# Performance work log

Hardware: AMD Instinct MI355X
Metric: run time of the kernel (lower is better)

The kernel has to match this reference:

```python
import jax, jax.numpy as jnp
import numpy as np

N = 50000
E = 800000
D_IN = 1000
D_H2 = 128  # h_dim * multiple
D_H = 16


def gat_conv(x, src, dst, W, attn_l, attn_r, bias, n):
    """DGL-style GATConv (no dropout, no activation). Returns [n, H, F]."""
    H, F = attn_l.shape
    feat = (x @ W).reshape(n, H, F)                      # [N,H,F]
    el = jnp.sum(feat * attn_l[None], axis=-1)           # [N,H]
    er = jnp.sum(feat * attn_r[None], axis=-1)           # [N,H]
    e = jax.nn.leaky_relu(el[src] + er[dst], 0.2)        # [E,H]
    emax = jax.ops.segment_max(e, dst, num_segments=n)   # [N,H] per-dst softmax max
    ee = jnp.exp(e - emax[dst])                          # [E,H]
    denom = jax.ops.segment_sum(ee, dst, num_segments=n) # [N,H]
    alpha = ee / denom[dst]                              # [E,H]
    msg = feat[src] * alpha[..., None]                   # [E,H,F]
    out = jax.ops.segment_sum(msg, dst, num_segments=n)  # [N,H,F]
    return out + bias.reshape(1, H, F)


def setup_inputs() -> dict:
    key = jax.random.key(0)
    ks = jax.random.split(key, 24)
    rn = lambda k, shp, s=0.05: (jax.random.normal(k, shp, dtype=jnp.float32) * s)
    inp = {
        "x": rn(ks[0], (N, D_IN), 1.0),
        "src": jax.random.randint(ks[1], (E,), 0, N, dtype=jnp.int32),
        "dst": jax.random.randint(ks[2], (E,), 0, N, dtype=jnp.int32),
        "W1": rn(ks[3], (D_IN, D_H2)),
        "al1": rn(ks[4], (1, D_H2)),
        "ar1": rn(ks[5], (1, D_H2)),
        "b1": jnp.zeros((D_H2,), jnp.float32),
        "W2": rn(ks[6], (D_H2, 2 * D_H2)),
        "al2": rn(ks[7], (2, D_H2)),
        "ar2": rn(ks[8], (2, D_H2)),
        "b2": jnp.zeros((2 * D_H2,), jnp.float32),
        "Wm": rn(ks[9], (D_H2, 2 * D_H)),
        "alm": rn(ks[10], (2, D_H)),
        "arm": rn(ks[11], (2, D_H)),
        "bm": jnp.zeros((2 * D_H,), jnp.float32),
        "Wv": rn(ks[12], (D_H2, 2 * D_H)),
        "alv": rn(ks[13], (2, D_H)),
        "arv": rn(ks[14], (2, D_H)),
        "bv": jnp.zeros((2 * D_H,), jnp.float32),
        "eps": rn(ks[15], (N, D_H), 1.0),
    }
    return inp


def reference(x, src, dst, W1, al1, ar1, b1, W2, al2, ar2, b2,
              Wm, alm, arm, bm, Wv, alv, arv, bv, eps):
    n = x.shape[0]
    o = gat_conv(x, src, dst, W1, al1, ar1, b1, n).mean(-2)           # [N,128]
    o = gat_conv(o, src, dst, W2, al2, ar2, b2, n).mean(-2) + o       # residual
    mean = gat_conv(o, src, dst, Wm, alm, arm, bm, n).mean(-2)        # [N,16]
    var = jnp.exp(gat_conv(o, src, dst, Wv, alv, arv, bv, n).mean(-2))
    z = mean + jnp.sqrt(var) * eps                                    # reparameterize
    return z, mean, var
```

## Files before the change

### kernel.cpp

```cpp
#include <hip/hip_runtime.h>
#include <hip/hip_bf16.h>
#include <math.h>

typedef unsigned short u16;
typedef unsigned int u32;
typedef __attribute__((ext_vector_type(8))) __bf16 bf16x8;
typedef __attribute__((ext_vector_type(4))) float f32x4;
typedef __attribute__((ext_vector_type(4))) u32 u32x4;

#define NNODES 50000
#define NEDGES 800000

__device__ __forceinline__ float bf2f(u16 u) {
    union { u32 i; float f; } v; v.i = ((u32)u) << 16; return v.f;
}
__device__ __forceinline__ u16 f2bf(float x) {
    union { float f; u32 i; } v; v.f = x;
    u32 r = v.i + 0x7fffu + ((v.i >> 16) & 1u);
    return (u16)(r >> 16);
}
__device__ __forceinline__ float lrelu(float x) { return x >= 0.f ? x : 0.2f * x; }

__global__ __launch_bounds__(256) void k_zero2(int* a, int* b, int count) {
    int i = blockIdx.x * 256 + threadIdx.x;
    if (i < count) { a[i] = 0; b[i] = 0; }
}

__global__ __launch_bounds__(256) void k_count(const int* __restrict__ dst, int* __restrict__ counts, int e) {
    int i = blockIdx.x * 256 + threadIdx.x;
    if (i < e) atomicAdd(&counts[dst[i]], 1);
}

__global__ __launch_bounds__(256) void k_scan1(const int* __restrict__ counts, int* __restrict__ row_ptr,
                                               int* __restrict__ bsums, int n) {
    __shared__ int tmp[256];
    int t = threadIdx.x, i = blockIdx.x * 256 + t;
    int v = (i < n) ? counts[i] : 0;
    tmp[t] = v; __syncthreads();
    for (int off = 1; off < 256; off <<= 1) {
        int x = 0; if (t >= off) x = tmp[t - off];
        __syncthreads(); tmp[t] += x; __syncthreads();
    }
    if (i < n) row_ptr[i] = tmp[t] - v;
    if (t == 255) bsums[blockIdx.x] = tmp[255];
}

__global__ __launch_bounds__(256) void k_scan2(int* bsums, int nb) {
    __shared__ int tmp[256];
    int t = threadIdx.x;
    int v = (t < nb) ? bsums[t] : 0;
    tmp[t] = v; __syncthreads();
    for (int off = 1; off < 256; off <<= 1) {
        int x = 0; if (t >= off) x = tmp[t - off];
        __syncthreads(); tmp[t] += x; __syncthreads();
    }
    if (t < nb) bsums[t] = tmp[t] - v;
}

__global__ __launch_bounds__(256) void k_scan3(int* __restrict__ row_ptr, const int* __restrict__ bsums,
                                               int n, int total) {
    int i = blockIdx.x * 256 + threadIdx.x;
    if (i < n) row_ptr[i] += bsums[blockIdx.x];
    if (i == 0) row_ptr[n] = total;
}

__global__ __launch_bounds__(256) void k_fill(const int* __restrict__ src, const int* __restrict__ dst,
                                              const int* __restrict__ row_ptr, int* __restrict__ cursor,
                                              int* __restrict__ esrc, int e) {
    int i = blockIdx.x * 256 + threadIdx.x;
    if (i < e) {
        int d = dst[i];
        int p = row_ptr[d] + atomicAdd(&cursor[d], 1);
        esrc[p] = src[i];
    }
}

__global__ __launch_bounds__(256) void k_prep(const float* __restrict__ W1, const float* __restrict__ W2,
                                              const float* __restrict__ Wm, const float* __restrict__ Wv,
                                              const float* __restrict__ al2, const float* __restrict__ ar2,
                                              const float* __restrict__ b2,
                                              u16* __restrict__ W1t, u16* __restrict__ Wct,
                                              u16* __restrict__ Bmvt,
                                              float* __restrict__ ul, float* __restrict__ ur,
                                              float* __restrict__ bmean) {
    int b = blockIdx.x, t = threadIdx.x;
    if (b < 500) {
        int i = b * 256 + t;
        int k = i >> 7, n = i & 127;
        W1t[(size_t)n * 1000 + k] = f2bf(W1[i]);
    } else if (b < 628) {
        int i = (b - 500) * 256 + t;
        int f = i >> 8, c = i & 255, h = c >> 7, k = c & 127;
        Wct[i] = f2bf(0.5f * W2[(size_t)k * 256 + h * 128 + f]);
    } else if (b == 628) {
        int h = t >> 7, k = t & 127;
        const float* wrow = W2 + (size_t)k * 256 + h * 128;
        const float* alh = al2 + h * 128;
        const float* arh = ar2 + h * 128;
        float sl = 0.f, sr = 0.f;
        for (int f = 0; f < 128; f += 4) {
            f32x4 w = *(const f32x4*)(wrow + f);
            f32x4 a = *(const f32x4*)(alh + f);
            f32x4 r = *(const f32x4*)(arh + f);
#pragma unroll
            for (int q = 0; q < 4; q++) { sl += w[q] * a[q]; sr += w[q] * r[q]; }
        }
        ul[t] = sl; ur[t] = sr;
        if (t < 128) bmean[t] = 0.5f * (b2[t] + b2[128 + t]);
    } else {
        for (int i = t; i < 64 * 128; i += 256) {
            int c = i >> 7, k = i & 127;
            Bmvt[i] = f2bf(c < 32 ? Wm[(size_t)k * 32 + c] : Wv[(size_t)k * 32 + (c - 32)]);
        }
    }
}

__device__ __forceinline__ void load_af(const float* __restrict__ arow, int k0, int K, bf16x8& a) {
    if (k0 + 8 <= K) {
        f32x4 a0 = *(const f32x4*)(arow + k0);
        f32x4 a1 = *(const f32x4*)(arow + k0 + 4);
#pragma unroll
        for (int j = 0; j < 4; j++) { a[j] = (__bf16)a0[j]; a[4 + j] = (__bf16)a1[j]; }
    } else {
#pragma unroll
        for (int j = 0; j < 8; j++) a[j] = (__bf16)0.f;
    }
}
__device__ __forceinline__ void load_af(const u16* __restrict__ arow, int k0, int K, bf16x8& a) {
    if (k0 + 8 <= K) a = *(const bf16x8*)(arow + k0);
    else {
#pragma unroll
        for (int j = 0; j < 8; j++) a[j] = (__bf16)0.f;
    }
}

template <typename AT, int MODE>
__global__ __launch_bounds__(256) void k_gemm_tiled(const AT* __restrict__ A, const u16* __restrict__ Bt,
                                                    u16* __restrict__ C, int M, int Nn, int K,
                                                    const float* __restrict__ bias,
                                                    const u16* __restrict__ resid,
                                                    const float* __restrict__ al,
                                                    const float* __restrict__ ar,
                                                    float* __restrict__ el, float* __restrict__ er) {
    __shared__ __align__(16) u16 lb[2][128 * 40];
    const int tid = threadIdx.x;
    const int wave = tid >> 6, lane = tid & 63;
    const int m = lane & 15, quad = lane >> 4;
    const int row0 = blockIdx.x * 64 + wave * 16;
    const int col0 = blockIdx.y * 128;

    f32x4 acc[8];
#pragma unroll
    for (int t = 0; t < 8; t++)
#pragma unroll
        for (int r = 0; r < 4; r++) acc[t][r] = 0.f;

    int arr = row0 + m; if (arr > M - 1) arr = M - 1;
    const AT* arow = A + (size_t)arr * K;
    const int scol = tid & 127;
    const int sseg = (tid >> 7) * 16;
    const u16* bcol = Bt + (size_t)(col0 + scol) * K;

    const int nsteps = (K + 31) >> 5;

#pragma unroll
    for (int p = 0; p < 2; ++p) {
        int kl = sseg + p * 8;
        u32x4 v = 0;
        if (kl < K) v = *(const u32x4*)(bcol + kl);
        *(u32x4*)&lb[0][scol * 40 + kl] = v;
    }
    bf16x8 acur, anext;
    load_af(arow, quad * 8, K, acur);
    __syncthreads();

    for (int s = 0; s < nsteps; ++s) {
        const int buf = s & 1;
        if (s + 1 < nsteps) {
            const int k0n = (s + 1) * 32;
            load_af(arow, k0n + quad * 8, K, anext);
#pragma unroll
            for (int p = 0; p < 2; ++p) {
                int kl = sseg + p * 8;
                u32x4 v = 0;
                if (k0n + kl < K) v = *(const u32x4*)(bcol + k0n + kl);
                *(u32x4*)&lb[buf ^ 1][scol * 40 + kl] = v;
            }
        }
#pragma unroll
        for (int t = 0; t < 8; ++t) {
            bf16x8 b = *(const bf16x8*)&lb[buf][(t * 16 + m) * 40 + quad * 8];
            acc[t] = __builtin_amdgcn_mfma_f32_16x16x32_bf16(acur, b, acc[t], 0, 0, 0);
        }
        acur = anext;
        __syncthreads();
    }

#pragma unroll
    for (int r = 0; r < 4; r++) {
        int row = row0 + quad * 4 + r;
        if (MODE == 0) {
            float pe = 0.f, pr = 0.f;
#pragma unroll
            for (int t = 0; t < 8; t++) {
                float a = acc[t][r];
                int c = col0 + t * 16 + m;
                pe += a * al[c]; pr += a * ar[c];
            }
#pragma unroll
            for (int off = 8; off; off >>= 1) { pe += __shfl_xor(pe, off); pr += __shfl_xor(pr, off); }
            if (m == 0 && row < M) { el[row] = pe; er[row] = pr; }
        }
#pragma unroll
        for (int t = 0; t < 8; t++) {
            int col = col0 + t * 16 + m;
            if (row < M) {
                float v = acc[t][r];
                if (MODE == 1) v += bias[col] + bf2f(resid[(size_t)row * Nn + col]);
                C[(size_t)row * Nn + col] = f2bf(v);
            }
        }
    }
}

__global__ __launch_bounds__(64) void k_gemmmv(const u16* __restrict__ A, const u16* __restrict__ Bt,
                                               u16* __restrict__ featm, u16* __restrict__ featv,
                                               const float* __restrict__ alm, const float* __restrict__ arm,
                                               const float* __restrict__ alv, const float* __restrict__ arv,
                                               float* __restrict__ elm, float* __restrict__ erm,
                                               float* __restrict__ elv, float* __restrict__ erv, int M) {
    int row0 = blockIdx.x * 16;
    int lane = threadIdx.x;
    int m = lane & 15, quad = lane >> 4;
    f32x4 acc[4];
#pragma unroll
    for (int t = 0; t < 4; t++)
#pragma unroll
        for (int r = 0; r < 4; r++) acc[t][r] = 0.f;

    const u16* arow = A + (size_t)(row0 + m) * 128 + quad * 8;
#pragma unroll
    for (int s = 0; s < 4; ++s) {
        bf16x8 a = *(const bf16x8*)(arow + s * 32);
#pragma unroll
        for (int t = 0; t < 4; t++) {
            bf16x8 b = *(const bf16x8*)(Bt + (size_t)(t * 16 + m) * 128 + s * 32 + quad * 8);
            acc[t] = __builtin_amdgcn_mfma_f32_16x16x32_bf16(a, b, acc[t], 0, 0, 0);
        }
    }
#pragma unroll
    for (int r = 0; r < 4; r++) {
        int row = row0 + quad * 4 + r;
#pragma unroll
        for (int t = 0; t < 4; t++) {
            float a = acc[t][r];
            const float* alp = (t < 2) ? alm : alv;
            const float* arp = (t < 2) ? arm : arv;
            float pe = a * alp[(t & 1) * 16 + m];
            float pr = a * arp[(t & 1) * 16 + m];
#pragma unroll
            for (int off = 8; off; off >>= 1) { pe += __shfl_xor(pe, off); pr += __shfl_xor(pr, off); }
            if (m == 0 && row < M) {
                float* elp = (t < 2) ? elm : elv;
                float* erp = (t < 2) ? erm : erv;
                elp[row * 2 + (t & 1)] = pe; erp[row * 2 + (t & 1)] = pr;
            }
            if (row < M) {
                u16 v = f2bf(a);
                if (t < 2) featm[(size_t)row * 32 + t * 16 + m] = v;
                else       featv[(size_t)row * 32 + (t - 2) * 16 + m] = v;
            }
        }
    }
}

__global__ __launch_bounds__(256) void k_agg1(const int* __restrict__ row_ptr, const int* __restrict__ esrc,
                                              const u16* __restrict__ feat, const float* __restrict__ el,
                                              const float* __restrict__ er, const float* __restrict__ bias,
                                              const float* __restrict__ ul, const float* __restrict__ ur,
                                              u16* __restrict__ o_bf, float* __restrict__ el2,
                                              float* __restrict__ er2, int n) {
    int node = blockIdx.x * 4 + (threadIdx.x >> 6);
    if (node >= n) return;
    int lane = threadIdx.x & 63;
    int beg = row_ptr[node], end = row_ptr[node + 1];
    float erd = er[node];
    float mx = -3.0e38f;
    for (int i = beg + lane; i < end; i += 64) mx = fmaxf(mx, el[esrc[i]]);
#pragma unroll
    for (int off = 32; off; off >>= 1) mx = fmaxf(mx, __shfl_xor(mx, off));
    float me = (end > beg) ? lrelu(mx + erd) : 0.f;
    float acc0 = 0.f, acc1 = 0.f, den = 0.f;
    for (int base = beg; base < end; base += 64) {
        int i = base + lane;
        float w = 0.f; int s = 0;
        if (i < end) { s = esrc[i]; w = expf(lrelu(el[s] + erd) - me); }
        den += w;
        int cnt = min(64, end - base);
        int j = 0;
        for (; j + 4 <= cnt; j += 4) {
            float w0 = __shfl(w, j), w1 = __shfl(w, j + 1), w2 = __shfl(w, j + 2), w3 = __shfl(w, j + 3);
            int s0 = __shfl(s, j), s1 = __shfl(s, j + 1), s2 = __shfl(s, j + 2), s3 = __shfl(s, j + 3);
            u32 p0 = ((const u32*)(feat + (size_t)s0 * 128))[lane];
            u32 p1 = ((const u32*)(feat + (size_t)s1 * 128))[lane];
            u32 p2 = ((const u32*)(feat + (size_t)s2 * 128))[lane];
            u32 p3 = ((const u32*)(feat + (size_t)s3 * 128))[lane];
            acc0 += w0 * bf2f((u16)(p0 & 0xffff)) + w1 * bf2f((u16)(p1 & 0xffff))
                  + w2 * bf2f((u16)(p2 & 0xffff)) + w3 * bf2f((u16)(p3 & 0xffff));
            acc1 += w0 * bf2f((u16)(p0 >> 16)) + w1 * bf2f((u16)(p1 >> 16))
                  + w2 * bf2f((u16)(p2 >> 16)) + w3 * bf2f((u16)(p3 >> 16));
        }
        for (; j < cnt; ++j) {
            float wj = __shfl(w, j);
            int sj = __shfl(s, j);
            u32 pv = ((const u32*)(feat + (size_t)sj * 128))[lane];
            acc0 += wj * bf2f((u16)(pv & 0xffff));
            acc1 += wj * bf2f((u16)(pv >> 16));
        }
    }
#pragma unroll
    for (int off = 32; off; off >>= 1) den += __shfl_xor(den, off);
    float inv = (den > 0.f) ? 1.f / den : 0.f;
    float o0 = acc0 * inv + bias[2 * lane];
    float o1 = acc1 * inv + bias[2 * lane + 1];
#pragma unroll
    for (int h = 0; h < 2; ++h) {
        float pe = o0 * ul[h * 128 + 2 * lane] + o1 * ul[h * 128 + 2 * lane + 1];
        float pr = o0 * ur[h * 128 + 2 * lane] + o1 * ur[h * 128 + 2 * lane + 1];
#pragma unroll
        for (int off = 32; off; off >>= 1) { pe += __shfl_xor(pe, off); pr += __shfl_xor(pr, off); }
        if (lane == 0) { el2[node * 2 + h] = pe; er2[node * 2 + h] = pr; }
    }
    u32 pv = (u32)f2bf(o0) | ((u32)f2bf(o1) << 16);
    ((u32*)(o_bf + (size_t)node * 128))[lane] = pv;
}

__global__ __launch_bounds__(256) void k_agg2o(const int* __restrict__ row_ptr, const int* __restrict__ esrc,
                                               const u16* __restrict__ o_in, const float* __restrict__ el,
                                               const float* __restrict__ er, u16* __restrict__ agg, int n) {
    int node = blockIdx.x * 4 + (threadIdx.x >> 6);
    if (node >= n) return;
    int lane = threadIdx.x & 63;
    int beg = row_ptr[node], end = row_ptr[node + 1];
    float er0 = er[node * 2], er1 = er[node * 2 + 1];
    float mx0 = -3.0e38f, mx1 = -3.0e38f;
    for (int i = beg + lane; i < end; i += 64) {
        int s = esrc[i];
        float2 e2 = *(const float2*)(el + 2 * s);
        mx0 = fmaxf(mx0, e2.x); mx1 = fmaxf(mx1, e2.y);
    }
#pragma unroll
    for (int off = 32; off; off >>= 1) { mx0 = fmaxf(mx0, __shfl_xor(mx0, off)); mx1 = fmaxf(mx1, __shfl_xor(mx1, off)); }
    float me0 = (end > beg) ? lrelu(mx0 + er0) : 0.f;
    float me1 = (end > beg) ? lrelu(mx1 + er1) : 0.f;
    float a00 = 0.f, a01 = 0.f, a10 = 0.f, a11 = 0.f, d0 = 0.f, d1 = 0.f;
    for (int base = beg; base < end; base += 64) {
        int i = base + lane;
        float w0 = 0.f, w1 = 0.f; int s = 0;
        if (i < end) {
            s = esrc[i];
            float2 e2 = *(const float2*)(el + 2 * s);
            w0 = expf(lrelu(e2.x + er0) - me0);
            w1 = expf(lrelu(e2.y + er1) - me1);
        }
        d0 += w0; d1 += w1;
        int cnt = min(64, end - base);
        int j = 0;
        for (; j + 4 <= cnt; j += 4) {
            float w0a = __shfl(w0, j), w0b = __shfl(w0, j + 1), w0c = __shfl(w0, j + 2), w0d = __shfl(w0, j + 3);
            float w1a = __shfl(w1, j), w1b = __shfl(w1, j + 1), w1c = __shfl(w1, j + 2), w1d = __shfl(w1, j + 3);
            int sa = __shfl(s, j), sb = __shfl(s, j + 1), sc = __shfl(s, j + 2), sd = __shfl(s, j + 3);
            u32 pa = ((const u32*)(o_in + (size_t)sa * 128))[lane];
            u32 pb = ((const u32*)(o_in + (size_t)sb * 128))[lane];
            u32 pc = ((const u32*)(o_in + (size_t)sc * 128))[lane];
            u32 pd = ((const u32*)(o_in + (size_t)sd * 128))[lane];
            float la = bf2f((u16)(pa & 0xffff)), ha = bf2f((u16)(pa >> 16));
            float lb = bf2f((u16)(pb & 0xffff)), hb = bf2f((u16)(pb >> 16));
            float lc = bf2f((u16)(pc & 0xffff)), hc = bf2f((u16)(pc >> 16));
            float ld = bf2f((u16)(pd & 0xffff)), hd = bf2f((u16)(pd >> 16));
            a00 += w0a * la + w0b * lb + w0c * lc + w0d * ld;
            a01 += w0a * ha + w0b * hb + w0c * hc + w0d * hd;
            a10 += w1a * la + w1b * lb + w1c * lc + w1d * ld;
            a11 += w1a * ha + w1b * hb + w1c * hc + w1d * hd;
        }
        for (; j < cnt; ++j) {
            float w0j = __shfl(w0, j), w1j = __shfl(w1, j);
            int sj = __shfl(s, j);
            u32 pv = ((const u32*)(o_in + (size_t)sj * 128))[lane];
            float lo = bf2f((u16)(pv & 0xffff)), hi = bf2f((u16)(pv >> 16));
            a00 += w0j * lo; a01 += w0j * hi;
            a10 += w1j * lo; a11 += w1j * hi;
        }
    }
#pragma unroll
    for (int off = 32; off; off >>= 1) { d0 += __shfl_xor(d0, off); d1 += __shfl_xor(d1, off); }
    float i0 = (d0 > 0.f) ? 1.f / d0 : 0.f, i1 = (d1 > 0.f) ? 1.f / d1 : 0.f;
    u32 p0 = (u32)f2bf(a00 * i0) | ((u32)f2bf(a01 * i0) << 16);
    u32 p1 = (u32)f2bf(a10 * i1) | ((u32)f2bf(a11 * i1) << 16);
    u32* aw = (u32*)(agg + (size_t)node * 256);
    aw[lane] = p0;
    aw[64 + lane] = p1;
}

__global__ __launch_bounds__(256) void k_aggmv(const int* __restrict__ row_ptr, const int* __restrict__ esrc,
                                               const u16* __restrict__ featm, const u16* __restrict__ featv,
                                               const float* __restrict__ elm, const float* __restrict__ erm,
                                               const float* __restrict__ elv, const float* __restrict__ erv,
                                               const float* __restrict__ bm, const float* __restrict__ bv,
                                               const float* __restrict__ eps, float* __restrict__ out, int n) {
    int node = blockIdx.x * 4 + (threadIdx.x >> 6);
    if (node >= n) return;
    int lane = threadIdx.x & 63;
    int f = lane & 15, h = (lane >> 4) & 1, tbl = lane >> 5;
    int beg = row_ptr[node], end = row_ptr[node + 1];
    float erm0 = erm[2 * node], erm1 = erm[2 * node + 1];
    float erv0 = erv[2 * node], erv1 = erv[2 * node + 1];
    float mm0 = -3.0e38f, mm1 = -3.0e38f, mv0 = -3.0e38f, mv1 = -3.0e38f;
    for (int i = beg + lane; i < end; i += 64) {
        int s = esrc[i];
        float2 em = *(const float2*)(elm + 2 * s);
        float2 ev = *(const float2*)(elv + 2 * s);
        mm0 = fmaxf(mm0, em.x); mm1 = fmaxf(mm1, em.y);
        mv0 = fmaxf(mv0, ev.x); mv1 = fmaxf(mv1, ev.y);
    }
#pragma unroll
    for (int off = 32; off; off >>= 1) {
        mm0 = fmaxf(mm0, __shfl_xor(mm0, off)); mm1 = fmaxf(mm1, __shfl_xor(mm1, off));
        mv0 = fmaxf(mv0, __shfl_xor(mv0, off)); mv1 = fmaxf(mv1, __shfl_xor(mv1, off));
    }
    float mem0 = (end > beg) ? lrelu(mm0 + erm0) : 0.f;
    float mem1 = (end > beg) ? lrelu(mm1 + erm1) : 0.f;
    float mev0 = (end > beg) ? lrelu(mv0 + erv0) : 0.f;
    float mev1 = (end > beg) ? lrelu(mv1 + erv1) : 0.f;

    const u16* ftp = tbl ? featv : featm;
    const int fidx = h * 16 + f;
    float accv = 0.f;
    float dm0 = 0.f, dm1 = 0.f, dv0 = 0.f, dv1 = 0.f;
    for (int base = beg; base < end; base += 64) {
        int i = base + lane;
        float wm0 = 0.f, wm1 = 0.f, wv0 = 0.f, wv1 = 0.f; int s = 0;
        if (i < end) {
            s = esrc[i];
            float2 em = *(const float2*)(elm + 2 * s);
            float2 ev = *(const float2*)(elv + 2 * s);
            wm0 = expf(lrelu(em.x + erm0) - mem0);
            wm1 = expf(lrelu(em.y + erm1) - mem1);
            wv0 = expf(lrelu(ev.x + erv0) - mev0);
            wv1 = expf(lrelu(ev.y + erv1) - mev1);
        }
        dm0 += wm0; dm1 += wm1; dv0 += wv0; dv1 += wv1;
        int cnt = min(64, end - base);
        for (int j = 0; j < cnt; ++j) {
            int sj = __shfl(s, j);
            float bm0 = __shfl(wm0, j);
            float bm1 = __shfl(wm1, j);
            float bv0 = __shfl(wv0, j);
            float bv1 = __shfl(wv1, j);
            float wj = tbl ? (h ? bv1 : bv0) : (h ? bm1 : bm0);
            accv += wj * bf2f(ftp[(size_t)sj * 32 + fidx]);
        }
    }
#pragma unroll
    for (int off = 32; off; off >>= 1) {
        dm0 += __shfl_xor(dm0, off); dm1 += __shfl_xor(dm1, off);
        dv0 += __shfl_xor(dv0, off); dv1 += __shfl_xor(dv1, off);
    }
    float den = tbl ? (h ? dv1 : dv0) : (h ? dm1 : dm0);
    float inv = (den > 0.f) ? 1.f / den : 0.f;
    float biasc = tbl ? bv[fidx] : bm[fidx];
    float outc = accv * inv + biasc;
    float hm = 0.5f * (outc + __shfl_xor(outc, 16));
    float meanv = __shfl(hm, f);
    float varp = __shfl(hm, 32 + f);
    if (lane < 16) {
        float var = expf(varp);
        float z = meanv + sqrtf(var) * eps[(size_t)node * 16 + f];
        size_t base = (size_t)node * 16 + f;
        out[base] = z;
        out[(size_t)NNODES * 16 + base] = meanv;
        out[(size_t)2 * NNODES * 16 + base] = var;
    }
}

extern "C" void kernel_launch(void* const* d_in, const int* in_sizes, int n_in,
                              void* d_out, int out_size, void* d_ws, size_t ws_size,
                              hipStream_t stream) {
    const int N = NNODES, E = NEDGES;
    const float* x   = (const float*)d_in[0];
    const int* src   = (const int*)d_in[1];
    const int* dst   = (const int*)d_in[2];
    const float* W1  = (const float*)d_in[3];
    const float* al1 = (const float*)d_in[4];
    const float* ar1 = (const float*)d_in[5];
    const float* b1  = (const float*)d_in[6];
    const float* W2  = (const float*)d_in[7];
    const float* al2 = (const float*)d_in[8];
    const float* ar2 = (const float*)d_in[9];
    const float* b2  = (const float*)d_in[10];
    const float* Wm  = (const float*)d_in[11];
    const float* alm = (const float*)d_in[12];
    const float* arm = (const float*)d_in[13];
    const float* bm  = (const float*)d_in[14];
    const float* Wv  = (const float*)d_in[15];
    const float* alv = (const float*)d_in[16];
    const float* arv = (const float*)d_in[17];
    const float* bv  = (const float*)d_in[18];
    const float* eps = (const float*)d_in[19];
    float* out = (float*)d_out;

    char* ws = (char*)d_ws;
    size_t off = 0;
    auto take = [&](size_t bytes) { size_t r = off; off += (bytes + 255) & ~(size_t)255; return r; };
    int* counts   = (int*)(ws + take((size_t)N * 4));
    int* cursor   = (int*)(ws + take((size_t)N * 4));
    int* row_ptr  = (int*)(ws + take((size_t)(N + 1) * 4));
    int* bsums    = (int*)(ws + take(256 * 4));
    int* esrc     = (int*)(ws + take((size_t)E * 4));
    u16* W1t      = (u16*)(ws + take((size_t)128 * 1000 * 2));
    u16* Wct      = (u16*)(ws + take((size_t)128 * 256 * 2));
    u16* Bmvt     = (u16*)(ws + take((size_t)64 * 128 * 2));
    float* ul2    = (float*)(ws + take(256 * 4));
    float* ur2    = (float*)(ws + take(256 * 4));
    float* bmean  = (float*)(ws + take(128 * 4));
    float* el1    = (float*)(ws + take((size_t)N * 4));
    float* er1    = (float*)(ws + take((size_t)N * 4));
    float* el2    = (float*)(ws + take((size_t)N * 2 * 4));
    float* er2    = (float*)(ws + take((size_t)N * 2 * 4));
    float* elm    = (float*)(ws + take((size_t)N * 2 * 4));
    float* erm    = (float*)(ws + take((size_t)N * 2 * 4));
    float* elv    = (float*)(ws + take((size_t)N * 2 * 4));
    float* erv    = (float*)(ws + take((size_t)N * 2 * 4));
    u16* o_bf     = (u16*)(ws + take((size_t)N * 128 * 2));
    u16* o2_bf    = (u16*)(ws + take((size_t)N * 128 * 2));
    u16* R        = (u16*)(ws + take((size_t)N * 256 * 2));
    u16* feat1    = R;
    u16* agg      = R;
    u16* featm    = R;
    u16* featv    = R + (size_t)N * 32;
    (void)ws_size; (void)n_in; (void)in_sizes; (void)out_size;

    const int nb = (N + 255) / 256;
    const int eb = (E + 255) / 256;
    const int wb = (N + 3) / 4;
    const int gb = (N + 63) / 64;

    k_prep<<<dim3(630), 256, 0, stream>>>(W1, W2, Wm, Wv, al2, ar2, b2, W1t, Wct, Bmvt, ul2, ur2, bmean);

    k_zero2<<<dim3(nb), 256, 0, stream>>>(counts, cursor, N);
    k_count<<<dim3(eb), 256, 0, stream>>>(dst, counts, E);
    k_scan1<<<dim3(nb), 256, 0, stream>>>(counts, row_ptr, bsums, N);
    k_scan2<<<dim3(1), 256, 0, stream>>>(bsums, nb);
    k_scan3<<<dim3(nb), 256, 0, stream>>>(row_ptr, bsums, N, E);
    k_fill<<<dim3(eb), 256, 0, stream>>>(src, dst, row_ptr, cursor, esrc, E);

    k_gemm_tiled<float, 0><<<dim3(gb, 1), 256, 0, stream>>>(x, W1t, feat1, N, 128, 1000,
                                                            nullptr, nullptr, al1, ar1, el1, er1);
    k_agg1<<<dim3(wb), 256, 0, stream>>>(row_ptr, esrc, feat1, el1, er1, b1, ul2, ur2,
                                         o_bf, el2, er2, N);

    k_agg2o<<<dim3(wb), 256, 0, stream>>>(row_ptr, esrc, o_bf, el2, er2, agg, N);
    k_gemm_tiled<u16, 1><<<dim3(gb, 1), 256, 0, stream>>>(agg, Wct, o2_bf, N, 128, 256,
                                                          bmean, o_bf, nullptr, nullptr, nullptr, nullptr);

    k_gemmmv<<<dim3(N / 16), 64, 0, stream>>>(o2_bf, Bmvt, featm, featv, alm, arm, alv, arv,
                                              elm, erm, elv, erv, N);
    k_aggmv<<<dim3(wb), 256, 0, stream>>>(row_ptr, esrc, featm, featv, elm, erm, elv, erv,
                                          bm, bv, eps, out, N);
}
```

Measured before the change: 650.7 us.

## Process two nodes per wavefront and drop softmax max pass in aggregations

Result: faster. 577.3 us (-11.3%).

```diff
diff --git a/kernel.cpp b/kernel.cpp
--- a/kernel.cpp
+++ b/kernel.cpp
@@ -7,6 +7,7 @@
 typedef __attribute__((ext_vector_type(8))) __bf16 bf16x8;
 typedef __attribute__((ext_vector_type(4))) float f32x4;
 typedef __attribute__((ext_vector_type(4))) u32 u32x4;
+typedef __attribute__((ext_vector_type(2))) u32 u32x2;
 
 #define NNODES 50000
 #define NEDGES 800000
@@ -224,7 +225,7 @@
 }
 
 __global__ __launch_bounds__(64) void k_gemmmv(const u16* __restrict__ A, const u16* __restrict__ Bt,
-                                               u16* __restrict__ featm, u16* __restrict__ featv,
+                                               u16* __restrict__ featmv,
                                                const float* __restrict__ alm, const float* __restrict__ arm,
                                                const float* __restrict__ alv, const float* __restrict__ arv,
                                                float* __restrict__ elm, float* __restrict__ erm,
@@ -265,11 +266,7 @@
                 float* erp = (t < 2) ? erm : erv;
                 elp[row * 2 + (t & 1)] = pe; erp[row * 2 + (t & 1)] = pr;
             }
-            if (row < M) {
-                u16 v = f2bf(a);
-                if (t < 2) featm[(size_t)row * 32 + t * 16 + m] = v;
-                else       featv[(size_t)row * 32 + (t - 2) * 16 + m] = v;
-            }
+            if (row < M) featmv[(size_t)row * 64 + t * 16 + m] = f2bf(a);
         }
     }
 }
@@ -280,206 +277,220 @@
                                               const float* __restrict__ ul, const float* __restrict__ ur,
                                               u16* __restrict__ o_bf, float* __restrict__ el2,
                                               float* __restrict__ er2, int n) {
-    int node = blockIdx.x * 4 + (threadIdx.x >> 6);
-    if (node >= n) return;
-    int lane = threadIdx.x & 63;
-    int beg = row_ptr[node], end = row_ptr[node + 1];
+    int wave = threadIdx.x >> 6, lane = threadIdx.x & 63;
+    int l = lane & 31;
+    int node = blockIdx.x * 8 + wave * 2 + (lane >> 5);
+    if (node >= n) node = n - 1;
+    int beg = row_ptr[node], deg = row_ptr[node + 1] - beg;
     float erd = er[node];
-    float mx = -3.0e38f;
-    for (int i = beg + lane; i < end; i += 64) mx = fmaxf(mx, el[esrc[i]]);
-#pragma unroll
-    for (int off = 32; off; off >>= 1) mx = fmaxf(mx, __shfl_xor(mx, off));
-    float me = (end > beg) ? lrelu(mx + erd) : 0.f;
-    float acc0 = 0.f, acc1 = 0.f, den = 0.f;
-    for (int base = beg; base < end; base += 64) {
-        int i = base + lane;
+    int degmax = max(deg, __shfl_xor(deg, 32));
+    const int srcb = lane & 32;
+    float acc0 = 0.f, acc1 = 0.f, acc2 = 0.f, acc3 = 0.f, den = 0.f;
+    for (int off0 = 0; off0 < degmax; off0 += 32) {
         float w = 0.f; int s = 0;
-        if (i < end) { s = esrc[i]; w = expf(lrelu(el[s] + erd) - me); }
+        if (off0 + l < deg) { s = esrc[beg + off0 + l]; w = expf(lrelu(el[s] + erd)); }
         den += w;
-        int cnt = min(64, end - base);
+        int cnt = min(32, degmax - off0);
         int j = 0;
         for (; j + 4 <= cnt; j += 4) {
-            float w0 = __shfl(w, j), w1 = __shfl(w, j + 1), w2 = __shfl(w, j + 2), w3 = __shfl(w, j + 3);
-            int s0 = __shfl(s, j), s1 = __shfl(s, j + 1), s2 = __shfl(s, j + 2), s3 = __shfl(s, j + 3);
-            u32 p0 = ((const u32*)(feat + (size_t)s0 * 128))[lane];
-            u32 p1 = ((const u32*)(feat + (size_t)s1 * 128))[lane];
-            u32 p2 = ((const u32*)(feat + (size_t)s2 * 128))[lane];
-            u32 p3 = ((const u32*)(feat + (size_t)s3 * 128))[lane];
-            acc0 += w0 * bf2f((u16)(p0 & 0xffff)) + w1 * bf2f((u16)(p1 & 0xffff))
-                  + w2 * bf2f((u16)(p2 & 0xffff)) + w3 * bf2f((u16)(p3 & 0xffff));
-            acc1 += w0 * bf2f((u16)(p0 >> 16)) + w1 * bf2f((u16)(p1 >> 16))
-                  + w2 * bf2f((u16)(p2 >> 16)) + w3 * bf2f((u16)(p3 >> 16));
+            int s0 = __shfl(s, srcb + j),     s1 = __shfl(s, srcb + j + 1);
+            int s2 = __shfl(s, srcb + j + 2), s3 = __shfl(s, srcb + j + 3);
+            float w0 = __shfl(w, srcb + j),     w1 = __shfl(w, srcb + j + 1);
+            float w2 = __shfl(w, srcb + j + 2), w3 = __shfl(w, srcb + j + 3);
+            u32x2 p0 = ((const u32x2*)(feat + (size_t)s0 * 128))[l];
+            u32x2 p1 = ((const u32x2*)(feat + (size_t)s1 * 128))[l];
+            u32x2 p2 = ((const u32x2*)(feat + (size_t)s2 * 128))[l];
+            u32x2 p3 = ((const u32x2*)(feat + (size_t)s3 * 128))[l];
+            acc0 += w0 * bf2f((u16)(p0.x & 0xffff)) + w1 * bf2f((u16)(p1.x & 0xffff))
+                  + w2 * bf2f((u16)(p2.x & 0xffff)) + w3 * bf2f((u16)(p3.x & 0xffff));
+            acc1 += w0 * bf2f((u16)(p0.x >> 16)) + w1 * bf2f((u16)(p1.x >> 16))
+                  + w2 * bf2f((u16)(p2.x >> 16)) + w3 * bf2f((u16)(p3.x >> 16));
+            acc2 += w0 * bf2f((u16)(p0.y & 0xffff)) + w1 * bf2f((u16)(p1.y & 0xffff))
+                  + w2 * bf2f((u16)(p2.y & 0xffff)) + w3 * bf2f((u16)(p3.y & 0xffff));
+            acc3 += w0 * bf2f((u16)(p0.y >> 16)) + w1 * bf2f((u16)(p1.y >> 16))
+                  + w2 * bf2f((u16)(p2.y >> 16)) + w3 * bf2f((u16)(p3.y >> 16));
         }
         for (; j < cnt; ++j) {
-            float wj = __shfl(w, j);
-            int sj = __shfl(s, j);
-            u32 pv = ((const u32*)(feat + (size_t)sj * 128))[lane];
-            acc0 += wj * bf2f((u16)(pv & 0xffff));
-            acc1 += wj * bf2f((u16)(pv >> 16));
-        }
-    }
-#pragma unroll
-    for (int off = 32; off; off >>= 1) den += __shfl_xor(den, off);
+            int sj = __shfl(s, srcb + j);
+            float wj = __shfl(w, srcb + j);
+            u32x2 pv = ((const u32x2*)(feat + (size_t)sj * 128))[l];
+            acc0 += wj * bf2f((u16)(pv.x & 0xffff));
+            acc1 += wj * bf2f((u16)(pv.x >> 16));
+            acc2 += wj * bf2f((u16)(pv.y & 0xffff));
+            acc3 += wj * bf2f((u16)(pv.y >> 16));
+        }
+    }
+#pragma unroll
+    for (int off = 16; off; off >>= 1) den += __shfl_xor(den, off);
     float inv = (den > 0.f) ? 1.f / den : 0.f;
-    float o0 = acc0 * inv + bias[2 * lane];
-    float o1 = acc1 * inv + bias[2 * lane + 1];
+    const int c0 = 4 * l;
+    float o0 = acc0 * inv + bias[c0];
+    float o1 = acc1 * inv + bias[c0 + 1];
+    float o2 = acc2 * inv + bias[c0 + 2];
+    float o3 = acc3 * inv + bias[c0 + 3];
 #pragma unroll
     for (int h = 0; h < 2; ++h) {
-        float pe = o0 * ul[h * 128 + 2 * lane] + o1 * ul[h * 128 + 2 * lane + 1];
-        float pr = o0 * ur[h * 128 + 2 * lane] + o1 * ur[h * 128 + 2 * lane + 1];
-#pragma unroll
-        for (int off = 32; off; off >>= 1) { pe += __shfl_xor(pe, off); pr += __shfl_xor(pr, off); }
-        if (lane == 0) { el2[node * 2 + h] = pe; er2[node * 2 + h] = pr; }
-    }
-    u32 pv = (u32)f2bf(o0) | ((u32)f2bf(o1) << 16);
-    ((u32*)(o_bf + (size_t)node * 128))[lane] = pv;
+        const float* ulh = ul + h * 128 + c0;
+        const float* urh = ur + h * 128 + c0;
+        float pe = o0 * ulh[0] + o1 * ulh[1] + o2 * ulh[2] + o3 * ulh[3];
+        float pr = o0 * urh[0] + o1 * urh[1] + o2 * urh[2] + o3 * urh[3];
+#pragma unroll
+        for (int off = 16; off; off >>= 1) { pe += __shfl_xor(pe, off); pr += __shfl_xor(pr, off); }
+        if (l == 0) { el2[node * 2 + h] = pe; er2[node * 2 + h] = pr; }
+    }
+    u32x2 pv;
+    pv.x = (u32)f2bf(o0) | ((u32)f2bf(o1) << 16);
+    pv.y = (u32)f2bf(o2) | ((u32)f2bf(o3) << 16);
+    ((u32x2*)(o_bf + (size_t)node * 128))[l] = pv;
 }
 
 __global__ __launch_bounds__(256) void k_agg2o(const int* __restrict__ row_ptr, const int* __restrict__ esrc,
                                                const u16* __restrict__ o_in, const float* __restrict__ el,
                                                const float* __restrict__ er, u16* __restrict__ agg, int n) {
-    int node = blockIdx.x * 4 + (threadIdx.x >> 6);
-    if (node >= n) return;
-    int lane = threadIdx.x & 63;
-    int beg = row_ptr[node], end = row_ptr[node + 1];
+    int wave = threadIdx.x >> 6, lane = threadIdx.x & 63;
+    int l = lane & 31;
+    int node = blockIdx.x * 8 + wave * 2 + (lane >> 5);
+    if (node >= n) node = n - 1;
+    int beg = row_ptr[node], deg = row_ptr[node + 1] - beg;
     float er0 = er[node * 2], er1 = er[node * 2 + 1];
-    float mx0 = -3.0e38f, mx1 = -3.0e38f;
-    for (int i = beg + lane; i < end; i += 64) {
-        int s = esrc[i];
-        float2 e2 = *(const float2*)(el + 2 * s);
-        mx0 = fmaxf(mx0, e2.x); mx1 = fmaxf(mx1, e2.y);
-    }
-#pragma unroll
-    for (int off = 32; off; off >>= 1) { mx0 = fmaxf(mx0, __shfl_xor(mx0, off)); mx1 = fmaxf(mx1, __shfl_xor(mx1, off)); }
-    float me0 = (end > beg) ? lrelu(mx0 + er0) : 0.f;
-    float me1 = (end > beg) ? lrelu(mx1 + er1) : 0.f;
-    float a00 = 0.f, a01 = 0.f, a10 = 0.f, a11 = 0.f, d0 = 0.f, d1 = 0.f;
-    for (int base = beg; base < end; base += 64) {
-        int i = base + lane;
+    int degmax = max(deg, __shfl_xor(deg, 32));
+    const int srcb = lane & 32;
+    float a00 = 0.f, a01 = 0.f, a02 = 0.f, a03 = 0.f;
+    float a10 = 0.f, a11 = 0.f, a12 = 0.f, a13 = 0.f;
+    float d0 = 0.f, d1 = 0.f;
+    for (int off0 = 0; off0 < degmax; off0 += 32) {
         float w0 = 0.f, w1 = 0.f; int s = 0;
-        if (i < end) {
-            s = esrc[i];
+        if (off0 + l < deg) {
+            s = esrc[beg + off0 + l];
             float2 e2 = *(const float2*)(el + 2 * s);
-            w0 = expf(lrelu(e2.x + er0) - me0);
-            w1 = expf(lrelu(e2.y + er1) - me1);
+            w0 = expf(lrelu(e2.x + er0));
+            w1 = expf(lrelu(e2.y + er1));
         }
         d0 += w0; d1 += w1;
-        int cnt = min(64, end - base);
+        int cnt = min(32, degmax - off0);
         int j = 0;
-        for (; j + 4 <= cnt; j += 4) {
-            float w0a = __shfl(w0, j), w0b = __shfl(w0, j + 1), w0c = __shfl(w0, j + 2), w0d = __shfl(w0, j + 3);
-            float w1a = __shfl(w1, j), w1b = __shfl(w1, j + 1), w1c = __shfl(w1, j + 2), w1d = __shfl(w1, j + 3);
-            int sa = __shfl(s, j), sb = __shfl(s, j + 1), sc = __shfl(s, j + 2), sd = __shfl(s, j + 3);
-            u32 pa = ((const u32*)(o_in + (size_t)sa * 128))[lane];
-            u32 pb = ((const u32*)(o_in + (size_t)sb * 128))[lane];
-            u32 pc = ((const u32*)(o_in + (size_t)sc * 128))[lane];
-            u32 pd = ((const u32*)(o_in + (size_t)sd * 128))[lane];
-            float la = bf2f((u16)(pa & 0xffff)), ha = bf2f((u16)(pa >> 16));
-            float lb = bf2f((u16)(pb & 0xffff)), hb = bf2f((u16)(pb >> 16));
-            float lc = bf2f((u16)(pc & 0xffff)), hc = bf2f((u16)(pc >> 16));
-            float ld = bf2f((u16)(pd & 0xffff)), hd = bf2f((u16)(pd >> 16));
-            a00 += w0a * la + w0b * lb + w0c * lc + w0d * ld;
-            a01 += w0a * ha + w0b * hb + w0c * hc + w0d * hd;
-            a10 += w1a * la + w1b * lb + w1c * lc + w1d * ld;
-            a11 += w1a * ha + w1b * hb + w1c * hc + w1d * hd;
+        for (; j + 2 <= cnt; j += 2) {
+            int sa = __shfl(s, srcb + j), sb = __shfl(s, srcb + j + 1);
+            float w0a = __shfl(w0, srcb + j), w0b = __shfl(w0, srcb + j + 1);
+            float w1a = __shfl(w1, srcb + j), w1b = __shfl(w1, srcb + j + 1);
+            u32x2 pa = ((const u32x2*)(o_in + (size_t)sa * 128))[l];
+            u32x2 pb = ((const u32x2*)(o_in + (size_t)sb * 128))[l];
+            float fa0 = bf2f((u16)(pa.x & 0xffff)), fa1 = bf2f((u16)(pa.x >> 16));
+            float fa2 = bf2f((u16)(pa.y & 0xffff)), fa3 = bf2f((u16)(pa.y >> 16));
+            float fb0 = bf2f((u16)(pb.x & 0xffff)), fb1 = bf2f((u16)(pb.x >> 16));
+            float fb2 = bf2f((u16)(pb.y & 0xffff)), fb3 = bf2f((u16)(pb.y >> 16));
+            a00 += w0a * fa0 + w0b * fb0;  a01 += w0a * fa1 + w0b * fb1;
+            a02 += w0a * fa2 + w0b * fb2;  a03 += w0a * fa3 + w0b * fb3;
+            a10 += w1a * fa0 + w1b * fb0;  a11 += w1a * fa1 + w1b * fb1;
+            a12 += w1a * fa2 + w1b * fb2;  a13 += w1a * fa3 + w1b * fb3;
         }
         for (; j < cnt; ++j) {
-            float w0j = __shfl(w0, j), w1j = __shfl(w1, j);
-            int sj = __shfl(s, j);
-            u32 pv = ((const u32*)(o_in + (size_t)sj * 128))[lane];
-            float lo = bf2f((u16)(pv & 0xffff)), hi = bf2f((u16)(pv >> 16));
-            a00 += w0j * lo; a01 += w0j * hi;
-            a10 += w1j * lo; a11 += w1j * hi;
-        }
-    }
-#pragma unroll
-    for (int off = 32; off; off >>= 1) { d0 += __shfl_xor(d0, off); d1 += __shfl_xor(d1, off); }
+            int sj = __shfl(s, srcb + j);
+            float w0j = __shfl(w0, srcb + j), w1j = __shfl(w1, srcb + j);
+            u32x2 pv = ((const u32x2*)(o_in + (size_t)sj * 128))[l];
+            float f0 = bf2f((u16)(pv.x & 0xffff)), f1 = bf2f((u16)(pv.x >> 16));
+            float f2 = bf2f((u16)(pv.y & 0xffff)), f3 = bf2f((u16)(pv.y >> 16));
+            a00 += w0j * f0; a01 += w0j * f1; a02 += w0j * f2; a03 += w0j * f3;
+            a10 += w1j * f0; a11 += w1j * f1; a12 += w1j * f2; a13 += w1j * f3;
+        }
+    }
+#pragma unroll
+    for (int off = 16; off; off >>= 1) { d0 += __shfl_xor(d0, off); d1 += __shfl_xor(d1, off); }
     float i0 = (d0 > 0.f) ? 1.f / d0 : 0.f, i1 = (d1 > 0.f) ? 1.f / d1 : 0.f;
-    u32 p0 = (u32)f2bf(a00 * i0) | ((u32)f2bf(a01 * i0) << 16);
-    u32 p1 = (u32)f2bf(a10 * i1) | ((u32)f2bf(a11 * i1) << 16);
-    u32* aw = (u32*)(agg + (size_t)node * 256);
-    aw[lane] = p0;
-    aw[64 + lane] = p1;
+    u32x2 p0, p1;
+    p0.x = (u32)f2bf(a00 * i0) | ((u32)f2bf(a01 * i0) << 16);
+    p0.y = (u32)f2bf(a02 * i0) | ((u32)f2bf(a03 * i0) << 16);
+    p1.x = (u32)f2bf(a10 * i1) | ((u32)f2bf(a11 * i1) << 16);
+    p1.y = (u32)f2bf(a12 * i1) | ((u32)f2bf(a13 * i1) << 16);
+    u32x2* aw = (u32x2*)(agg + (size_t)node * 256);
+    aw[l] = p0;
+    aw[32 + l] = p1;
 }
 
 __global__ __launch_bounds__(256) void k_aggmv(const int* __restrict__ row_ptr, const int* __restrict__ esrc,
-                                               const u16* __restrict__ featm, const u16* __restrict__ featv,
+                                               const u16* __restrict__ featmv,
                                                const float* __restrict__ elm, const float* __restrict__ erm,
                                                const float* __restrict__ elv, const float* __restrict__ erv,
                                                const float* __restrict__ bm, const float* __restrict__ bv,
                                                const float* __restrict__ eps, float* __restrict__ out, int n) {
-    int node = blockIdx.x * 4 + (threadIdx.x >> 6);
-    if (node >= n) return;
-    int lane = threadIdx.x & 63;
-    int f = lane & 15, h = (lane >> 4) & 1, tbl = lane >> 5;
-    int beg = row_ptr[node], end = row_ptr[node + 1];
+    int wave = threadIdx.x >> 6, lane = threadIdx.x & 63;
+    int l = lane & 31;
+    int node = blockIdx.x * 8 + wave * 2 + (lane >> 5);
+    if (node >= n) node = n - 1;
+    int tbl = l >> 4, h = (l >> 3) & 1;
+    int beg = row_ptr[node], deg = row_ptr[node + 1] - beg;
     float erm0 = erm[2 * node], erm1 = erm[2 * node + 1];
     float erv0 = erv[2 * node], erv1 = erv[2 * node + 1];
-    float mm0 = -3.0e38f, mm1 = -3.0e38f, mv0 = -3.0e38f, mv1 = -3.0e38f;
-    for (int i = beg + lane; i < end; i += 64) {
-        int s = esrc[i];
-        float2 em = *(const float2*)(elm + 2 * s);
-        float2 ev = *(const float2*)(elv + 2 * s);
-        mm0 = fmaxf(mm0, em.x); mm1 = fmaxf(mm1, em.y);
-        mv0 = fmaxf(mv0, ev.x); mv1 = fmaxf(mv1, ev.y);
-    }
-#pragma unroll
-    for (int off = 32; off; off >>= 1) {
-        mm0 = fmaxf(mm0, __shfl_xor(mm0, off)); mm1 = fmaxf(mm1, __shfl_xor(mm1, off));
-        mv0 = fmaxf(mv0, __shfl_xor(mv0, off)); mv1 = fmaxf(mv1, __shfl_xor(mv1, off));
-    }
-    float mem0 = (end > beg) ? lrelu(mm0 + erm0) : 0.f;
-    float mem1 = (end > beg) ? lrelu(mm1 + erm1) : 0.f;
-    float mev0 = (end > beg) ? lrelu(mv0 + erv0) : 0.f;
-    float mev1 = (end > beg) ? lrelu(mv1 + erv1) : 0.f;
-
-    const u16* ftp = tbl ? featv : featm;
-    const int fidx = h * 16 + f;
-    float accv = 0.f;
+    int degmax = max(deg, __shfl_xor(deg, 32));
+    const int srcb = lane & 32;
+    float acc0 = 0.f, acc1 = 0.f;
     float dm0 = 0.f, dm1 = 0.f, dv0 = 0.f, dv1 = 0.f;
-    for (int base = beg; base < end; base += 64) {
-        int i = base + lane;
+    for (int off0 = 0; off0 < degmax; off0 += 32) {
         float wm0 = 0.f, wm1 = 0.f, wv0 = 0.f, wv1 = 0.f; int s = 0;
-        if (i < end) {
-            s = esrc[i];
+        if (off0 + l < deg) {
+            s = esrc[beg + off0 + l];
             float2 em = *(const float2*)(elm + 2 * s);
             float2 ev = *(const float2*)(elv + 2 * s);
-            wm0 = expf(lrelu(em.x + erm0) - mem0);
-            wm1 = expf(lrelu(em.y + erm1) - mem1);
-            wv0 = expf(lrelu(ev.x + erv0) - mev0);
-            wv1 = expf(lrelu(ev.y + erv1) - mev1);
+            wm0 = expf(lrelu(em.x + erm0));
+            wm1 = expf(lrelu(em.y + erm1));
+            wv0 = expf(lrelu(ev.x + erv0));
+            wv1 = expf(lrelu(ev.y + erv1));
         }
         dm0 += wm0; dm1 += wm1; dv0 += wv0; dv1 += wv1;
-        int cnt = min(64, end - base);
-        for (int j = 0; j < cnt; ++j) {
-            int sj = __shfl(s, j);
-            float bm0 = __shfl(wm0, j);
-            float bm1 = __shfl(wm1, j);
-            float bv0 = __shfl(wv0, j);
-            float bv1 = __shfl(wv1, j);
-            float wj = tbl ? (h ? bv1 : bv0) : (h ? bm1 : bm0);
-            accv += wj * bf2f(ftp[(size_t)sj * 32 + fidx]);
-        }
-    }
-#pragma unroll
-    for (int off = 32; off; off >>= 1) {
+        int cnt = min(32, degmax - off0);
+        int j = 0;
+        for (; j + 2 <= cnt; j += 2) {
+            int sa = __shfl(s, srcb + j), sb = __shfl(s, srcb + j + 1);
+            float am0 = __shfl(wm0, srcb + j), bm0_ = __shfl(wm0, srcb + j + 1);
+            float am1 = __shfl(wm1, srcb + j), bm1_ = __shfl(wm1, srcb + j + 1);
+            float av0 = __shfl(wv0, srcb + j), bv0_ = __shfl(wv0, srcb + j + 1);
+            float av1 = __shfl(wv1, srcb + j), bv1_ = __shfl(wv1, srcb + j + 1);
+            float wa = tbl ? (h ? av1 : av0) : (h ? am1 : am0);
+            float wb = tbl ? (h ? bv1_ : bv0_) : (h ? bm1_ : bm0_);
+            u32 pa = ((const u32*)(featmv + (size_t)sa * 64))[l];
+            u32 pb = ((const u32*)(featmv + (size_t)sb * 64))[l];
+            acc0 += wa * bf2f((u16)(pa & 0xffff)) + wb * bf2f((u16)(pb & 0xffff));
+            acc1 += wa * bf2f((u16)(pa >> 16)) + wb * bf2f((u16)(pb >> 16));
+        }
+        for (; j < cnt; ++j) {
+            int sj = __shfl(s, srcb + j);
+            float b0 = __shfl(wm0, srcb + j);
+            float b1 = __shfl(wm1, srcb + j);
+            float b2 = __shfl(wv0, srcb + j);
+            float b3 = __shfl(wv1, srcb + j);
+            float wj = tbl ? (h ? b3 : b2) : (h ? b1 : b0);
+            u32 pv = ((const u32*)(featmv + (size_t)sj * 64))[l];
+            acc0 += wj * bf2f((u16)(pv & 0xffff));
+            acc1 += wj * bf2f((u16)(pv >> 16));
+        }
+    }
+#pragma unroll
+    for (int off = 16; off; off >>= 1) {
         dm0 += __shfl_xor(dm0, off); dm1 += __shfl_xor(dm1, off);
         dv0 += __shfl_xor(dv0, off); dv1 += __shfl_xor(dv1, off);
     }
     float den = tbl ? (h ? dv1 : dv0) : (h ? dm1 : dm0);
     float inv = (den > 0.f) ? 1.f / den : 0.f;
-    float biasc = tbl ? bv[fidx] : bm[fidx];
-    float outc = accv * inv + biasc;
-    float hm = 0.5f * (outc + __shfl_xor(outc, 16));
-    float meanv = __shfl(hm, f);
-    float varp = __shfl(hm, 32 + f);
-    if (lane < 16) {
-        float var = expf(varp);
-        float z = meanv + sqrtf(var) * eps[(size_t)node * 16 + f];
-        size_t base = (size_t)node * 16 + f;
-        out[base] = z;
-        out[(size_t)NNODES * 16 + base] = meanv;
-        out[(size_t)2 * NNODES * 16 + base] = var;
+    const int fidx0 = (2 * l) & 31;
+    float bias0 = tbl ? bv[fidx0] : bm[fidx0];
+    float bias1 = tbl ? bv[fidx0 + 1] : bm[fidx0 + 1];
+    float outc0 = acc0 * inv + bias0;
+    float outc1 = acc1 * inv + bias1;
+    float hm0 = 0.5f * (outc0 + __shfl_xor(outc0, 8));
+    float hm1 = 0.5f * (outc1 + __shfl_xor(outc1, 8));
+    int srcv = srcb + 16 + (l & 7);
+    float vp0 = __shfl(hm0, srcv);
+    float vp1 = __shfl(hm1, srcv);
+    if (l < 8) {
+        int f0 = 2 * l;
+        float var0 = expf(vp0), var1 = expf(vp1);
+        float2 e2 = *(const float2*)(eps + (size_t)node * 16 + f0);
+        float z0 = hm0 + sqrtf(var0) * e2.x;
+        float z1 = hm1 + sqrtf(var1) * e2.y;
+        size_t base = (size_t)node * 16 + f0;
+        *(float2*)(out + base) = make_float2(z0, z1);
+        *(float2*)(out + (size_t)NNODES * 16 + base) = make_float2(hm0, hm1);
+        *(float2*)(out + (size_t)2 * NNODES * 16 + base) = make_float2(var0, var1);
     }
 }
 
@@ -536,13 +547,12 @@
     u16* R        = (u16*)(ws + take((size_t)N * 256 * 2));
     u16* feat1    = R;
     u16* agg      = R;
-    u16* featm    = R;
-    u16* featv    = R + (size_t)N * 32;
+    u16* featmv   = R;
     (void)ws_size; (void)n_in; (void)in_sizes; (void)out_size;
 
     const int nb = (N + 255) / 256;
     const int eb = (E + 255) / 256;
-    const int wb = (N + 3) / 4;
+    const int wb8 = (N + 7) / 8;
     const int gb = (N + 63) / 64;
 
     k_prep<<<dim3(630), 256, 0, stream>>>(W1, W2, Wm, Wv, al2, ar2, b2, W1t, Wct, Bmvt, ul2, ur2, bmean);
@@ -556,15 +566,15 @@
 
     k_gemm_tiled<float, 0><<<dim3(gb, 1), 256, 0, stream>>>(x, W1t, feat1, N, 128, 1000,
                                                             nullptr, nullptr, al1, ar1, el1, er1);
-    k_agg1<<<dim3(wb), 256, 0, stream>>>(row_ptr, esrc, feat1, el1, er1, b1, ul2, ur2,
-                                         o_bf, el2, er2, N);
-
-    k_agg2o<<<dim3(wb), 256, 0, stream>>>(row_ptr, esrc, o_bf, el2, er2, agg, N);
+    k_agg1<<<dim3(wb8), 256, 0, stream>>>(row_ptr, esrc, feat1, el1, er1, b1, ul2, ur2,
+                                          o_bf, el2, er2, N);
+
+    k_agg2o<<<dim3(wb8), 256, 0, stream>>>(row_ptr, esrc, o_bf, el2, er2, agg, N);
     k_gemm_tiled<u16, 1><<<dim3(gb, 1), 256, 0, stream>>>(agg, Wct, o2_bf, N, 128, 256,
                                                           bmean, o_bf, nullptr, nullptr, nullptr, nullptr);
 
-    k_gemmmv<<<dim3(N / 16), 64, 0, stream>>>(o2_bf, Bmvt, featm, featv, alm, arm, alv, arv,
+    k_gemmmv<<<dim3(N / 16), 64, 0, stream>>>(o2_bf, Bmvt, featmv, alm, arm, alv, arv,
                                               elm, erm, elv, erv, N);
-    k_aggmv<<<dim3(wb), 256, 0, stream>>>(row_ptr, esrc, featm, featv, elm, erm, elv, erv,
-                                          bm, bv, eps, out, N);
-}
+    k_aggmv<<<dim3(wb8), 256, 0, stream>>>(row_ptr, esrc, featmv, elm, erm, elv, erv,
+                                           bm, bv, eps, out, N);
+}
```
